# Kernel optimization log

Measured on AMD Instinct MI355X. Metric: run time of the kernel, lower is better.

Reference implementation:

```python
import jax, jax.numpy as jnp
import numpy as np

HIDDEN = 450
DEPTH = 6
ATOM_FDIM = 35          # len(ELEM_LIST)+6+5+1
BOND_FDIM = 5
MAX_NB = 15
N_ATOMS = 20000
N_BONDS = 40000
N_MESS = 16000          # tree messages (row 0 is the zero padding slot)
N_MOLS = 1000


def _linear_init(key, out_dim, in_dim):
    s = 1.0 / np.sqrt(in_dim)
    return jax.random.uniform(key, (out_dim, in_dim), jnp.float32, -s, s)


def setup_inputs() -> dict:
    key = jax.random.key(0)
    ks = jax.random.split(key, 9)
    total_msg = N_MESS + N_BONDS
    fatoms = jax.random.normal(ks[0], (N_ATOMS, ATOM_FDIM), jnp.float32)
    fbonds = jax.random.normal(ks[1], (N_BONDS, ATOM_FDIM + BOND_FDIM), jnp.float32)
    agraph = jax.random.randint(ks[2], (N_ATOMS, MAX_NB), 0, total_msg, jnp.int32)
    bgraph = jax.random.randint(ks[3], (N_BONDS, MAX_NB), 0, total_msg, jnp.int32)
    tree_message = jax.random.normal(ks[4], (N_MESS, HIDDEN), jnp.float32)
    tree_message = tree_message.at[0].set(0.0)  # index 0 = padding message
    # uniform scope: N_MOLS molecules of N_ATOMS//N_MOLS atoms each
    mol_ids = jnp.repeat(jnp.arange(N_MOLS, dtype=jnp.int32), N_ATOMS // N_MOLS)
    W_i = _linear_init(ks[5], HIDDEN, ATOM_FDIM + BOND_FDIM)
    W_h = _linear_init(ks[6], HIDDEN, HIDDEN)
    W_o = _linear_init(ks[7], HIDDEN, ATOM_FDIM + HIDDEN)
    s = 1.0 / np.sqrt(ATOM_FDIM + HIDDEN)
    b_o = jax.random.uniform(ks[8], (HIDDEN,), jnp.float32, -s, s)
    return {"fatoms": fatoms, "fbonds": fbonds, "agraph": agraph, "bgraph": bgraph,
            "mol_ids": mol_ids, "n_mols": N_MOLS, "tree_message": tree_message,
            "W_i": W_i, "W_h": W_h, "W_o": W_o, "b_o": b_o}


def reference(fatoms, fbonds, agraph, bgraph, mol_ids, n_mols, tree_message,
              W_i, W_h, W_o, b_o):
    binput = fbonds @ W_i.T                       # [B, H]
    graph_message = jax.nn.relu(binput)
    for _ in range(DEPTH - 1):                    # static depth loop
        message = jnp.concatenate([tree_message, graph_message], axis=0)  # [M+B, H]
        nei_message = message[bgraph].sum(axis=1)  # gather [B, MAX_NB, H] -> [B, H]
        graph_message = jax.nn.relu(binput + nei_message @ W_h.T)
    message = jnp.concatenate([tree_message, graph_message], axis=0)
    nei_message = message[agraph].sum(axis=1)      # [A, H]
    ainput = jnp.concatenate([fatoms, nei_message], axis=1)  # [A, ATOM_FDIM+H]
    atom_hiddens = jax.nn.relu(ainput @ W_o.T + b_o)          # [A, H]
    # mean over each molecule's atoms (scope)
    sums = jax.ops.segment_sum(atom_hiddens, mol_ids, num_segments=n_mols)
    counts = jax.ops.segment_sum(jnp.ones((atom_hiddens.shape[0], 1), atom_hiddens.dtype),
                                 mol_ids, num_segments=n_mols)
    return sums / counts
```

## Files before the change

kernel.cpp:

```cpp
#include <hip/hip_runtime.h>

#define HIDDEN 450
#define MAX_NB 15
#define N_ATOMS 20000
#define N_BONDS 40000
#define N_MESS  16000
#define N_MOLS  1000
#define KPAD    512
#define MSTRIDE 456
#define FSTRIDE 64

typedef unsigned int uint;
typedef unsigned short ushort;
typedef __bf16 bf16x8 __attribute__((ext_vector_type(8)));
typedef float  f32x4  __attribute__((ext_vector_type(4)));

__device__ __forceinline__ ushort f2bf(float f) {
    uint u = __builtin_bit_cast(uint, f);
    u += 0x7fffu + ((u >> 16) & 1u);
    return (ushort)(u >> 16);
}
__device__ __forceinline__ float bfhi(uint w) {
    return __builtin_bit_cast(float, w & 0xffff0000u);
}
__device__ __forceinline__ float bflo(uint w) {
    return __builtin_bit_cast(float, w << 16);
}


__global__ __launch_bounds__(256) void pack_tree(const float* __restrict__ tree,
                                                 ushort* __restrict__ tbuf) {
    const int r = blockIdx.x, t = threadIdx.x;
    if (t < 228) {
        uint p = 0;
        if (t < 225) {
            const float2 v = *(const float2*)&tree[(size_t)r * HIDDEN + 2 * t];
            p = (uint)f2bf(v.x) | ((uint)f2bf(v.y) << 16);
        }
        ((uint*)(tbuf + (size_t)r * MSTRIDE))[t] = p;
    }
}

__global__ __launch_bounds__(256) void pack_bonds(const float* __restrict__ fbonds,
                                                  ushort* __restrict__ Abuf) {
    const int r = blockIdx.x * 4 + (threadIdx.x >> 6);
    const int t = threadIdx.x & 63;
    if (r >= N_BONDS) return;
    Abuf[(size_t)r * FSTRIDE + t] = (t < 40) ? f2bf(fbonds[(size_t)r * 40 + t])
                                             : (ushort)0;
}

__global__ __launch_bounds__(256) void pack_atoms(const float* __restrict__ fatoms,
                                                  ushort* __restrict__ Aout) {
    const int r = blockIdx.x * 4 + (threadIdx.x >> 6);
    const int t = threadIdx.x & 63;
    if (r >= N_ATOMS) return;
    Aout[(size_t)r * FSTRIDE + t] = (t < 35) ? f2bf(fatoms[(size_t)r * 35 + t])
                                             : (ushort)0;
}

__global__ __launch_bounds__(256) void pack_w(const float* __restrict__ W_i,
                                              const float* __restrict__ W_h,
                                              const float* __restrict__ W_o,
                                              ushort* __restrict__ Wcat,
                                              ushort* __restrict__ Wocat) {
    const int n = blockIdx.x;
    for (int c = threadIdx.x; c < KPAD; c += 256) {
        float v = 0.0f, vo = 0.0f;
        if (n < HIDDEN) {
            if (c < 40)       v = W_i[(size_t)n * 40 + c];
            else if (c < 490) v = W_h[(size_t)n * HIDDEN + (c - 40)];
            if (c < 35)       vo = W_o[(size_t)n * 485 + c];
            else if (c >= 40 && c < 490) vo = W_o[(size_t)n * 485 + 35 + (c - 40)];
        }
        Wcat [(size_t)n * KPAD + c] = f2bf(v);
        Wocat[(size_t)n * KPAD + c] = f2bf(vo);
    }
}

__global__ __launch_bounds__(256) void precompute_base(const int* __restrict__ g,
                                                       const ushort* __restrict__ tbuf,
                                                       ushort* __restrict__ base,
                                                       int nrows) {
    const int r_raw = blockIdx.x * 4 + (threadIdx.x >> 6);
    const int lane = threadIdx.x & 63;
    if (r_raw >= nrows) return;
    const int r = __builtin_amdgcn_readfirstlane(r_raw);
    const int* gr = g + (size_t)r * MAX_NB;
    const ushort* p[MAX_NB];
#pragma unroll
    for (int j = 0; j < MAX_NB; ++j) {
        const int idx = gr[j];
        p[j] = tbuf + (size_t)((idx < N_MESS) ? idx : 0) * MSTRIDE;
    }
    if (lane >= 57) return;
    const int off = lane * 8;
    uint4 w[MAX_NB];
#pragma unroll
    for (int j = 0; j < MAX_NB; ++j) w[j] = *(const uint4*)(p[j] + off);
    float acc[8] = {};
#pragma unroll
    for (int j = 0; j < MAX_NB; ++j) {
        acc[0] += bflo(w[j].x); acc[1] += bfhi(w[j].x);
        acc[2] += bflo(w[j].y); acc[3] += bfhi(w[j].y);
        acc[4] += bflo(w[j].z); acc[5] += bfhi(w[j].z);
        acc[6] += bflo(w[j].w); acc[7] += bfhi(w[j].w);
    }
    uint4 o;
    o.x = (uint)f2bf(acc[0]) | ((uint)f2bf(acc[1]) << 16);
    o.y = (uint)f2bf(acc[2]) | ((uint)f2bf(acc[3]) << 16);
    o.z = (uint)f2bf(acc[4]) | ((uint)f2bf(acc[5]) << 16);
    o.w = (uint)f2bf(acc[6]) | ((uint)f2bf(acc[7]) << 16);
    *(uint4*)(base + (size_t)r * MSTRIDE + off) = o;
}

template <int KT, int AST>
__global__ __launch_bounds__(256, 2) void mfma_gemm0(
    const ushort* __restrict__ A, int M,
    const ushort* __restrict__ W,
    ushort* __restrict__ gout, int mtiles) {
    __shared__ ushort At[64 * KT * 32];
    const int tid = threadIdx.x;
    const int id  = blockIdx.x;
    const int b     = id & 7;
    const int n_blk = (id >> 3) & 1;
    const int m_blk = (id >> 4) * 8 + b;
    if (m_blk >= mtiles) return;
    const int m0 = m_blk * 64, n0 = n_blk * 256;
    const int CPR = KT * 4;

    {
        const int srow = tid >> 2;
        const int c0   = tid & 3;
        const ushort* gsrc = A + (size_t)min(m0 + srow, M - 1) * AST;
        ushort* lrow = At + srow * (KT * 32);
#pragma unroll
        for (int c = c0; c < CPR; c += 4) {
            const uint4 v = *(const uint4*)(gsrc + c * 8);
            *(uint4*)&lrow[(c ^ (srow & 7)) * 8] = v;
        }
    }
    __syncthreads();

    const int lane = tid & 63;
    const int wave = tid >> 6;
    const int wn = wave * 64;
    const int lr = lane & 15;
    const int lk = lane >> 4;

    size_t woff[4];
#pragma unroll
    for (int s = 0; s < 4; ++s)
        woff[s] = (size_t)(n0 + wn + s * 16 + lr) * KPAD + lk * 8;

    f32x4 acc[4][4];
#pragma unroll
    for (int i = 0; i < 4; ++i)
#pragma unroll
        for (int j = 0; j < 4; ++j) acc[i][j] = (f32x4){0.f, 0.f, 0.f, 0.f};

    bf16x8 wa[4], wb[4], afa[4];
#pragma unroll
    for (int s = 0; s < 4; ++s) wa[s] = *(const bf16x8*)&W[woff[s]];
#pragma unroll
    for (int s = 0; s < 4; ++s)
        wb[s] = (KT > 1) ? *(const bf16x8*)&W[woff[s] + 32] : wa[s];
#pragma unroll
    for (int mt = 0; mt < 4; ++mt) {
        const int row = mt * 16 + lr;
        afa[mt] = *(const bf16x8*)&At[(row * CPR + (lk ^ (row & 7))) * 8];
    }

#pragma unroll
    for (int i = 0; i < KT; ++i) {
        bf16x8 wc[4], afb[4];
        if (i + 2 < KT) {
#pragma unroll
            for (int s = 0; s < 4; ++s)
                wc[s] = *(const bf16x8*)&W[woff[s] + (size_t)(i + 2) * 32];
        }
        if (i + 1 < KT) {
#pragma unroll
            for (int mt = 0; mt < 4; ++mt) {
                const int row = mt * 16 + lr;
                const int chunk = (((i + 1) * 4 + lk)) ^ (row & 7);
                afb[mt] = *(const bf16x8*)&At[(row * CPR + chunk) * 8];
            }
        }
#pragma unroll
        for (int mt = 0; mt < 4; ++mt)
#pragma unroll
            for (int nt = 0; nt < 4; ++nt)
                acc[mt][nt] = __builtin_amdgcn_mfma_f32_16x16x32_bf16(
                    afa[mt], wa[nt], acc[mt][nt], 0, 0, 0);
        if (i + 1 < KT) {
#pragma unroll
            for (int s = 0; s < 4; ++s) wa[s] = wb[s];
#pragma unroll
            for (int mt = 0; mt < 4; ++mt) afa[mt] = afb[mt];
        }
        if (i + 2 < KT) {
#pragma unroll
            for (int s = 0; s < 4; ++s) wb[s] = wc[s];
        }
    }

    const int col_l = lane & 15;
    const int rbase = (lane >> 4) * 4;
#pragma unroll
    for (int mt = 0; mt < 4; ++mt) {
        const int mbase = m0 + mt * 16 + rbase;
#pragma unroll
        for (int nt = 0; nt < 4; ++nt) {
            const int n = n0 + wn + nt * 16 + col_l;
#pragma unroll
            for (int reg = 0; reg < 4; ++reg) {
                const int m = mbase + reg;
                if (m >= M) continue;
                if (n < HIDDEN)
                    gout[(size_t)m * MSTRIDE + n] = f2bf(fmaxf(acc[mt][nt][reg], 0.0f));
                else if (n < MSTRIDE)
                    gout[(size_t)m * MSTRIDE + n] = 0;
            }
        }
    }
}

template <int MODE>
__global__ __launch_bounds__(512, 4) void fused_gg(
    const int* __restrict__ g,
    const ushort* __restrict__ base,
    const ushort* __restrict__ gin,
    const ushort* __restrict__ zrow,
    const ushort* __restrict__ feat,
    const ushort* __restrict__ W,
    const float* __restrict__ bias, const int* __restrict__ mol_ids,
    ushort* __restrict__ gout, float* __restrict__ aout, int M) {
    __shared__ ushort At[64 * KPAD];
    const int tid  = threadIdx.x;
    const int lane = tid & 63;
    const int wave = tid >> 6;
    const int m0 = blockIdx.x * 64;

#pragma unroll 1
    for (int rr = 0; rr < 8; ++rr) {
        const int r = (wave << 3) | rr;
        const int m = __builtin_amdgcn_readfirstlane(min(m0 + r, M - 1));
        const int sw = r & 7;
        ushort* lrow = At + r * KPAD;
        const int* gr = g + (size_t)m * MAX_NB;
        const ushort* p[MAX_NB];
#pragma unroll
        for (int j = 0; j < MAX_NB; ++j) {
            const int row = gr[j] - N_MESS;
            p[j] = (row >= 0) ? gin + (size_t)row * MSTRIDE : zrow;
        }
        if (lane < 57) {
            const int off = lane * 8;
            uint4 w[MAX_NB];
#pragma unroll
            for (int j = 0; j < MAX_NB; ++j) w[j] = *(const uint4*)(p[j] + off);
            const uint4 b = *(const uint4*)(base + (size_t)m * MSTRIDE + off);
            float acc[8];
            acc[0] = bflo(b.x); acc[1] = bfhi(b.x);
            acc[2] = bflo(b.y); acc[3] = bfhi(b.y);
            acc[4] = bflo(b.z); acc[5] = bfhi(b.z);
            acc[6] = bflo(b.w); acc[7] = bfhi(b.w);
#pragma unroll
            for (int j = 0; j < MAX_NB; ++j) {
                acc[0] += bflo(w[j].x); acc[1] += bfhi(w[j].x);
                acc[2] += bflo(w[j].y); acc[3] += bfhi(w[j].y);
                acc[4] += bflo(w[j].z); acc[5] += bfhi(w[j].z);
                acc[6] += bflo(w[j].w); acc[7] += bfhi(w[j].w);
            }
            uint4 o;
            o.x = (uint)f2bf(acc[0]) | ((uint)f2bf(acc[1]) << 16);
            o.y = (uint)f2bf(acc[2]) | ((uint)f2bf(acc[3]) << 16);
            o.z = (uint)f2bf(acc[4]) | ((uint)f2bf(acc[5]) << 16);
            o.w = (uint)f2bf(acc[6]) | ((uint)f2bf(acc[7]) << 16);
            *(uint4*)&lrow[((5 + lane) ^ sw) * 8] = o;
        } else {
            const int c = (lane < 62) ? (lane - 57) : lane;
            uint4 v = (uint4){0u, 0u, 0u, 0u};
            if (lane < 62)
                v = *(const uint4*)(feat + (size_t)m * FSTRIDE + (lane - 57) * 8);
            *(uint4*)&lrow[(c ^ sw) * 8] = v;
        }
    }
    __syncthreads();

    const int wn = wave * 64;
    const int lr = lane & 15;
    const int lk = lane >> 4;

    size_t woff[4];
#pragma unroll
    for (int s = 0; s < 4; ++s)
        woff[s] = (size_t)(wn + s * 16 + lr) * KPAD + lk * 8;

    f32x4 acc[4][4];
#pragma unroll
    for (int i = 0; i < 4; ++i)
#pragma unroll
        for (int j = 0; j < 4; ++j) acc[i][j] = (f32x4){0.f, 0.f, 0.f, 0.f};

    bf16x8 wa[4], wb[4], afa[4];
#pragma unroll
    for (int s = 0; s < 4; ++s) wa[s] = *(const bf16x8*)&W[woff[s]];
#pragma unroll
    for (int s = 0; s < 4; ++s) wb[s] = *(const bf16x8*)&W[woff[s] + 32];
#pragma unroll
    for (int mt = 0; mt < 4; ++mt) {
        const int row = mt * 16 + lr;
        afa[mt] = *(const bf16x8*)&At[(row * 64 + (lk ^ (row & 7))) * 8];
    }

#pragma unroll
    for (int i = 0; i < 16; ++i) {
        bf16x8 wc[4], afb[4];
        if (i + 2 < 16) {
#pragma unroll
            for (int s = 0; s < 4; ++s)
                wc[s] = *(const bf16x8*)&W[woff[s] + (size_t)(i + 2) * 32];
        }
        if (i + 1 < 16) {
#pragma unroll
            for (int mt = 0; mt < 4; ++mt) {
                const int row = mt * 16 + lr;
                const int chunk = (((i + 1) * 4 + lk)) ^ (row & 7);
                afb[mt] = *(const bf16x8*)&At[(row * 64 + chunk) * 8];
            }
        }
#pragma unroll
        for (int mt = 0; mt < 4; ++mt)
#pragma unroll
            for (int nt = 0; nt < 4; ++nt)
                acc[mt][nt] = __builtin_amdgcn_mfma_f32_16x16x32_bf16(
                    afa[mt], wa[nt], acc[mt][nt], 0, 0, 0);
        if (i + 1 < 16) {
#pragma unroll
            for (int s = 0; s < 4; ++s) wa[s] = wb[s];
#pragma unroll
            for (int mt = 0; mt < 4; ++mt) afa[mt] = afb[mt];
        }
        if (i + 2 < 16) {
#pragma unroll
            for (int s = 0; s < 4; ++s) wb[s] = wc[s];
        }
    }

    const int col_l = lane & 15;
    const int rbase = (lane >> 4) * 4;
#pragma unroll
    for (int mt = 0; mt < 4; ++mt) {
        const int mbase = m0 + mt * 16 + rbase;
        int mol[4];
        if (MODE == 1) {
#pragma unroll
            for (int reg = 0; reg < 4; ++reg)
                mol[reg] = mol_ids[min(mbase + reg, M - 1)];
        }
#pragma unroll
        for (int nt = 0; nt < 4; ++nt) {
            const int n = wn + nt * 16 + col_l;
            if (MODE == 0) {
#pragma unroll
                for (int reg = 0; reg < 4; ++reg) {
                    const int m = mbase + reg;
                    if (m >= M) continue;
                    if (n < HIDDEN)
                        gout[(size_t)m * MSTRIDE + n] = f2bf(fmaxf(acc[mt][nt][reg], 0.0f));
                    else if (n < MSTRIDE)
                        gout[(size_t)m * MSTRIDE + n] = 0;
                }
            } else {
                if (n >= HIDDEN) continue;
                const float bsum = bias[n];
                float run = 0.0f;
                int cur = mol[0];
#pragma unroll
                for (int reg = 0; reg < 4; ++reg) {
                    const float v = (mbase + reg < M)
                        ? fmaxf(acc[mt][nt][reg] + bsum, 0.0f) : 0.0f;
                    if (mol[reg] != cur) {
                        atomicAdd(&aout[(size_t)cur * HIDDEN + n], run);
                        cur = mol[reg];
                        run = 0.0f;
                    }
                    run += v;
                }
                atomicAdd(&aout[(size_t)cur * HIDDEN + n], run);
            }
        }
    }
}

__global__ __launch_bounds__(256) void count_atoms(const int* __restrict__ mol_ids,
                                                   float* __restrict__ counts) {
    const int a = blockIdx.x * 256 + threadIdx.x;
    if (a < N_ATOMS) atomicAdd(&counts[mol_ids[a]], 1.0f);
}
__global__ __launch_bounds__(256) void div_counts(float* __restrict__ out,
                                                  const float* __restrict__ counts) {
    const int i = blockIdx.x * 256 + threadIdx.x;
    if (i < N_MOLS * HIDDEN) out[i] = out[i] / counts[i / HIDDEN];
}

extern "C" void kernel_launch(void* const* d_in, const int* in_sizes, int n_in,
                              void* d_out, int out_size, void* d_ws, size_t ws_size,
                              hipStream_t stream) {
    const float* fatoms  = (const float*)d_in[0];
    const float* fbonds  = (const float*)d_in[1];
    const int*   agraph  = (const int*)d_in[2];
    const int*   bgraph  = (const int*)d_in[3];
    const int*   mol_ids = (const int*)d_in[4];
    const float* tree    = (const float*)d_in[6];
    const float* W_i     = (const float*)d_in[7];
    const float* W_h     = (const float*)d_in[8];
    const float* W_o     = (const float*)d_in[9];
    const float* b_o     = (const float*)d_in[10];
    float* out = (float*)d_out;

    ushort* zrow   = (ushort*)d_ws;
    ushort* Abuf   = zrow   + 512;
    ushort* Aout   = Abuf   + (size_t)N_BONDS * FSTRIDE;
    ushort* gmsgA  = Aout   + (size_t)N_ATOMS * FSTRIDE;
    ushort* gmsgB  = gmsgA  + (size_t)N_BONDS * MSTRIDE;
    ushort* tbuf   = gmsgB  + (size_t)N_BONDS * MSTRIDE;
    ushort* Wcat   = tbuf   + (size_t)N_MESS  * MSTRIDE;
    ushort* Wocat  = Wcat   + (size_t)KPAD * KPAD;
    ushort* base_b = Wocat  + (size_t)KPAD * KPAD;
    ushort* base_a = base_b + (size_t)N_BONDS * MSTRIDE;
    float*  counts = (float*)(base_a + (size_t)N_ATOMS * MSTRIDE);

    (void)hipMemsetAsync(d_out, 0, (size_t)N_MOLS * HIDDEN * sizeof(float), stream);
    (void)hipMemsetAsync(counts, 0, N_MOLS * sizeof(float), stream);
    (void)hipMemsetAsync(zrow, 0, 512 * sizeof(ushort), stream);

    const dim3 blk(256);
    pack_tree <<<N_MESS, blk, 0, stream>>>(tree, tbuf);
    pack_bonds<<<(N_BONDS + 3) / 4, blk, 0, stream>>>(fbonds, Abuf);
    pack_atoms<<<(N_ATOMS + 3) / 4, blk, 0, stream>>>(fatoms, Aout);
    pack_w    <<<KPAD, blk, 0, stream>>>(W_i, W_h, W_o, Wcat, Wocat);
    precompute_base<<<(N_BONDS + 3) / 4, blk, 0, stream>>>(bgraph, tbuf, base_b, N_BONDS);
    precompute_base<<<(N_ATOMS + 3) / 4, blk, 0, stream>>>(agraph, tbuf, base_a, N_ATOMS);

    const int mtB = (N_BONDS + 63) / 64;
    const int mtA = (N_ATOMS + 63) / 64;
    const dim3 gB0(((mtB + 7) / 8) * 16);

    mfma_gemm0<2, FSTRIDE><<<gB0, blk, 0, stream>>>(Abuf, N_BONDS, Wcat, gmsgA, mtB);

    ushort* cur = gmsgA;
    ushort* nxt = gmsgB;
    const dim3 blk2(512);
    for (int it = 0; it < 5; ++it) {
        fused_gg<0><<<mtB, blk2, 0, stream>>>(bgraph, base_b, cur, zrow, Abuf, Wcat,
                                              nullptr, nullptr, nxt, nullptr, N_BONDS);
        ushort* t = cur; cur = nxt; nxt = t;
    }
    fused_gg<1><<<mtA, blk2, 0, stream>>>(agraph, base_a, cur, zrow, Aout, Wocat,
                                          b_o, mol_ids, nullptr, out, N_ATOMS);

    count_atoms<<<(N_ATOMS + 255) / 256, blk, 0, stream>>>(mol_ids, counts);
    div_counts <<<(N_MOLS * HIDDEN + 255) / 256, blk, 0, stream>>>(out, counts);
}
```

Measured before the change: 840.5 us.

## Halve fused gather-GEMM row tile to 32 and simplify the MFMA prefetch pipeline

Cuts the per-block row tile of the fused gather+GEMM kernel from 64 to 32 rows, halving LDS use and accumulator registers and doubling the grid. The launch-bounds occupancy hint is raised from 4 to 6 blocks. The two-deep weight prefetch and the register prefetch of A fragments are replaced by one-step weight prefetch with A fragments loaded from LDS inside each iteration. Each block now reads the full weight matrix for half as many rows, so weight traffic per output doubles, and LDS latency is less hidden, in exchange for more concurrent blocks to hide the gather latency.

```diff
diff --git a/kernel.cpp b/kernel.cpp
--- a/kernel.cpp
+++ b/kernel.cpp
@@ -9,6 +9,7 @@
 #define KPAD    512
 #define MSTRIDE 456
 #define FSTRIDE 64
+#define BM      32
 
 typedef unsigned int uint;
 typedef unsigned short ushort;
@@ -227,7 +228,7 @@
 }
 
 template <int MODE>
-__global__ __launch_bounds__(512, 4) void fused_gg(
+__global__ __launch_bounds__(512, 6) void fused_gg(
     const int* __restrict__ g,
     const ushort* __restrict__ base,
     const ushort* __restrict__ gin,
@@ -236,15 +237,15 @@
     const ushort* __restrict__ W,
     const float* __restrict__ bias, const int* __restrict__ mol_ids,
     ushort* __restrict__ gout, float* __restrict__ aout, int M) {
-    __shared__ ushort At[64 * KPAD];
+    __shared__ ushort At[BM * KPAD];
     const int tid  = threadIdx.x;
     const int lane = tid & 63;
     const int wave = tid >> 6;
-    const int m0 = blockIdx.x * 64;
-
-#pragma unroll 1
-    for (int rr = 0; rr < 8; ++rr) {
-        const int r = (wave << 3) | rr;
+    const int m0 = blockIdx.x * BM;
+
+#pragma unroll 2
+    for (int rr = 0; rr < 4; ++rr) {
+        const int r = (wave << 2) | rr;
         const int m = __builtin_amdgcn_readfirstlane(min(m0 + r, M - 1));
         const int sw = r & 7;
         ushort* lrow = At + r * KPAD;
@@ -298,41 +299,32 @@
     for (int s = 0; s < 4; ++s)
         woff[s] = (size_t)(wn + s * 16 + lr) * KPAD + lk * 8;
 
-    f32x4 acc[4][4];
-#pragma unroll
-    for (int i = 0; i < 4; ++i)
+    f32x4 acc[2][4];
+#pragma unroll
+    for (int i = 0; i < 2; ++i)
 #pragma unroll
         for (int j = 0; j < 4; ++j) acc[i][j] = (f32x4){0.f, 0.f, 0.f, 0.f};
 
-    bf16x8 wa[4], wb[4], afa[4];
+    bf16x8 wa[4], wb[4];
 #pragma unroll
     for (int s = 0; s < 4; ++s) wa[s] = *(const bf16x8*)&W[woff[s]];
-#pragma unroll
-    for (int s = 0; s < 4; ++s) wb[s] = *(const bf16x8*)&W[woff[s] + 32];
-#pragma unroll
-    for (int mt = 0; mt < 4; ++mt) {
-        const int row = mt * 16 + lr;
-        afa[mt] = *(const bf16x8*)&At[(row * 64 + (lk ^ (row & 7))) * 8];
-    }
 
 #pragma unroll
     for (int i = 0; i < 16; ++i) {
-        bf16x8 wc[4], afb[4];
-        if (i + 2 < 16) {
+        if (i + 1 < 16) {
 #pragma unroll
             for (int s = 0; s < 4; ++s)
-                wc[s] = *(const bf16x8*)&W[woff[s] + (size_t)(i + 2) * 32];
-        }
-        if (i + 1 < 16) {
-#pragma unroll
-            for (int mt = 0; mt < 4; ++mt) {
-                const int row = mt * 16 + lr;
-                const int chunk = (((i + 1) * 4 + lk)) ^ (row & 7);
-                afb[mt] = *(const bf16x8*)&At[(row * 64 + chunk) * 8];
-            }
-        }
-#pragma unroll
-        for (int mt = 0; mt < 4; ++mt)
+                wb[s] = *(const bf16x8*)&W[woff[s] + (size_t)(i + 1) * 32];
+        }
+        bf16x8 afa[2];
+#pragma unroll
+        for (int mt = 0; mt < 2; ++mt) {
+            const int row = mt * 16 + lr;
+            const int chunk = (i * 4 + lk) ^ (row & 7);
+            afa[mt] = *(const bf16x8*)&At[(row * 64 + chunk) * 8];
+        }
+#pragma unroll
+        for (int mt = 0; mt < 2; ++mt)
 #pragma unroll
             for (int nt = 0; nt < 4; ++nt)
                 acc[mt][nt] = __builtin_amdgcn_mfma_f32_16x16x32_bf16(
@@ -340,19 +332,13 @@
         if (i + 1 < 16) {
 #pragma unroll
             for (int s = 0; s < 4; ++s) wa[s] = wb[s];
-#pragma unroll
-            for (int mt = 0; mt < 4; ++mt) afa[mt] = afb[mt];
-        }
-        if (i + 2 < 16) {
-#pragma unroll
-            for (int s = 0; s < 4; ++s) wb[s] = wc[s];
         }
     }
 
     const int col_l = lane & 15;
     const int rbase = (lane >> 4) * 4;
 #pragma unroll
-    for (int mt = 0; mt < 4; ++mt) {
+    for (int mt = 0; mt < 2; ++mt) {
         const int mbase = m0 + mt * 16 + rbase;
         int mol[4];
         if (MODE == 1) {
@@ -446,20 +432,21 @@
     precompute_base<<<(N_ATOMS + 3) / 4, blk, 0, stream>>>(agraph, tbuf, base_a, N_ATOMS);
 
     const int mtB = (N_BONDS + 63) / 64;
-    const int mtA = (N_ATOMS + 63) / 64;
     const dim3 gB0(((mtB + 7) / 8) * 16);
 
     mfma_gemm0<2, FSTRIDE><<<gB0, blk, 0, stream>>>(Abuf, N_BONDS, Wcat, gmsgA, mtB);
 
+    const int fgB = (N_BONDS + BM - 1) / BM;
+    const int fgA = (N_ATOMS + BM - 1) / BM;
     ushort* cur = gmsgA;
     ushort* nxt = gmsgB;
     const dim3 blk2(512);
     for (int it = 0; it < 5; ++it) {
-        fused_gg<0><<<mtB, blk2, 0, stream>>>(bgraph, base_b, cur, zrow, Abuf, Wcat,
+        fused_gg<0><<<fgB, blk2, 0, stream>>>(bgraph, base_b, cur, zrow, Abuf, Wcat,
                                               nullptr, nullptr, nxt, nullptr, N_BONDS);
         ushort* t = cur; cur = nxt; nxt = t;
     }
-    fused_gg<1><<<mtA, blk2, 0, stream>>>(agraph, base_a, cur, zrow, Aout, Wocat,
+    fused_gg<1><<<fgA, blk2, 0, stream>>>(agraph, base_a, cur, zrow, Aout, Wocat,
                                           b_o, mol_ids, nullptr, out, N_ATOMS);
 
     count_atoms<<<(N_ATOMS + 255) / 256, blk, 0, stream>>>(mol_ids, counts);
```

After: 912.2 us. +8.5%, slower.
